# Optimization experiments

Hardware: AMD Instinct MI355X
Metric: run time of the kernel (lower is better)

## Reference

```python
import jax, jax.numpy as jnp
import numpy as np

B, S, D, H, L, V, F = 4, 2048, 512, 8, 4, 32000, 512
EPS = 1e-3  # keras BatchNormalization default epsilon


def setup_inputs() -> dict:
    key = jax.random.key(0)
    ks = jax.random.split(key, 32)
    n = lambda k, shp, sc=0.02: (jax.random.normal(k, shp, jnp.float32) * sc)
    inp = {
        "sequence": jax.random.randint(ks[0], (B, S), 0, V, dtype=jnp.int32),
        # padding mask: 1 for kept tokens, 0 for padded; broadcast over [B,h,S,S]
        "padding_mask": (jax.random.uniform(ks[1], (B, 1, 1, S)) > 0.1).astype(jnp.float32),
        "pos_embeddings": n(ks[2], (S, D), 1.0),
        "emb": n(ks[3], (V, D), 1.0),
        "wq": n(ks[4], (L, D, D)), "bq": jnp.zeros((L, D), jnp.float32),
        "wk": n(ks[5], (L, D, D)), "bk": jnp.zeros((L, D), jnp.float32),
        "wv": n(ks[6], (L, D, D)), "bv": jnp.zeros((L, D), jnp.float32),
        "wo": n(ks[7], (L, D, D)), "bo": jnp.zeros((L, D), jnp.float32),
        "an_gamma": 1.0 + n(ks[8], (L, D)), "an_beta": n(ks[9], (L, D)),
        "an_mean": n(ks[10], (L, D), 0.1), "an_var": 0.5 + jax.random.uniform(ks[11], (L, D)),
        "d1_w": n(ks[12], (L, D, F)), "d1_b": jnp.zeros((L, F), jnp.float32),
        "d2_w": n(ks[13], (L, F, D)), "d2_b": jnp.zeros((L, D), jnp.float32),
        "fn_gamma": 1.0 + n(ks[14], (L, D)), "fn_beta": n(ks[15], (L, D)),
        "fn_mean": n(ks[16], (L, D), 0.1), "fn_var": 0.5 + jax.random.uniform(ks[17], (L, D)),
    }
    return inp


def _bn(x, gamma, beta, mean, var):
    # keras BatchNormalization in inference mode (moving statistics), axis=-1
    return (x - mean) * jax.lax.rsqrt(var + EPS) * gamma + beta


def reference(sequence, padding_mask, pos_embeddings, emb,
              wq, bq, wk, bk, wv, bv, wo, bo,
              an_gamma, an_beta, an_mean, an_var,
              d1_w, d1_b, d2_w, d2_b,
              fn_gamma, fn_beta, fn_mean, fn_var):
    b, s = sequence.shape
    nlayers, d, _ = wq.shape
    h = H
    dk = d // h
    scale = 1.0 / jnp.sqrt(jnp.float32(dk))

    x = emb[sequence] + pos_embeddings[:s, :]  # [B,S,D]

    def split_heads(t):  # [B,S,D] -> [B,h,S,dk]
        return t.reshape(b, s, h, dk).transpose(0, 2, 1, 3)

    for i in range(nlayers):
        q = split_heads(x @ wq[i] + bq[i])
        k = split_heads(x @ wk[i] + bk[i])
        v = split_heads(x @ wv[i] + bv[i])
        score = jnp.einsum('bhqd,bhkd->bhqk', q, k) * scale  # [B,h,S,S]
        if padding_mask is not None:
            score = score * padding_mask
            score = jnp.where(score == 0, jnp.float32(-1e9), score)
        align = jax.nn.softmax(score, axis=-1)
        ctx = jnp.einsum('bhqk,bhkd->bhqd', align, v)
        ctx = ctx.transpose(0, 2, 1, 3).reshape(b, s, d)
        heads = ctx @ wo[i] + bo[i]
        sub = _bn(x + heads, an_gamma[i], an_beta[i], an_mean[i], an_var[i])
        ffn = jax.nn.relu(sub @ d1_w[i] + d1_b[i]) @ d2_w[i] + d2_b[i]
        x = _bn(sub + ffn, fn_gamma[i], fn_beta[i], fn_mean[i], fn_var[i])
    return x
```

## Files before the change

kernel.cpp:

```cpp
#include <hip/hip_runtime.h>
#include <stdint.h>
#include <stddef.h>

constexpr int BB = 4, SS = 2048, DD = 512, HH = 8, LL = 4;
constexpr int NTOK = BB * SS;
constexpr float BN_EPS = 1e-3f;

using bh = __bf16;
typedef __bf16 bf16x8 __attribute__((ext_vector_type(8)));
typedef float  f32x4  __attribute__((ext_vector_type(4)));

#define DEV __device__ __forceinline__
#define WAITVM(n) asm volatile("s_waitcnt vmcnt(" #n ")" ::: "memory")
#define WAITLGKM0 asm volatile("s_waitcnt lgkmcnt(0)" ::: "memory")

DEV void gload_lds16(const void* g, void* l) {
    __builtin_amdgcn_global_load_lds(
        (const __attribute__((address_space(1))) void*)g,
        (__attribute__((address_space(3))) void*)l, 16, 0, 0);
}

__global__ void wprep(const float* __restrict__ in, bh* __restrict__ out, int ostride) {
    __shared__ float t[32][33];
    const float* ip = in + (size_t)blockIdx.z * DD * DD;
    bh* op = out + (size_t)blockIdx.z * ostride;
    const int r0 = blockIdx.y * 32, c0 = blockIdx.x * 32;
    const int tx = threadIdx.x, ty = threadIdx.y;
    #pragma unroll
    for (int i = ty; i < 32; i += 8) t[i][tx] = ip[(size_t)(r0 + i) * DD + c0 + tx];
    __syncthreads();
    #pragma unroll
    for (int i = ty; i < 32; i += 8) op[(size_t)(c0 + i) * DD + r0 + tx] = (bh)t[tx][i];
}

__global__ void maskprep(const float* __restrict__ mask, float* __restrict__ mb) {
    const int i = ((int)blockIdx.x * 256 + threadIdx.x) * 4;
    const float4 m4 = *(const float4*)(mask + i);
    float4 o;
    o.x = (m4.x == 0.f) ? -1e30f : 0.f;
    o.y = (m4.y == 0.f) ? -1e30f : 0.f;
    o.z = (m4.z == 0.f) ? -1e30f : 0.f;
    o.w = (m4.w == 0.f) ? -1e30f : 0.f;
    *(float4*)(mb + i) = o;
}

__global__ void embed_k(const int* __restrict__ seq, const float* __restrict__ emb,
                        const float* __restrict__ pos, bh* __restrict__ xb) {
    const int m = blockIdx.x;
    const int s = m & (SS - 1);
    const int tok = seq[m];
    const int d = threadIdx.x * 4;
    const float4 e  = *(const float4*)(emb + (size_t)tok * DD + d);
    const float4 pz = *(const float4*)(pos + (size_t)s * DD + d);
    union { bh h[4]; uint64_t u; } pk;
    pk.h[0] = (bh)(e.x + pz.x); pk.h[1] = (bh)(e.y + pz.y);
    pk.h[2] = (bh)(e.z + pz.z); pk.h[3] = (bh)(e.w + pz.w);
    *(uint64_t*)(xb + (size_t)m * DD + d) = pk.u;
}

template <int EP, bool WF32>
__global__ __launch_bounds__(256, 4)
void gemm64(const bh* __restrict__ A, const bh* __restrict__ Bt,
            const float* __restrict__ bias, bh* __restrict__ outb,
            const bh* __restrict__ resb, float* __restrict__ Xo,
            const float* __restrict__ gamma, const float* __restrict__ beta,
            const float* __restrict__ mean, const float* __restrict__ var) {
    constexpr int BK = 64, NKT = DD / BK;
    __shared__ __align__(16) bh As[2][64 * BK];
    __shared__ __align__(16) bh Bs[2][64 * BK];

    const int tid = threadIdx.x;
    const int w = tid >> 6, lane = tid & 63;
    const int l15 = lane & 15, l4 = lane >> 4;
    const int i = (int)blockIdx.x;
    const int xcd = i & 7, j = i >> 3;
    const int bm = xcd * 16 + (j >> 3);
    const int bn = j & 7;
    const int m0 = bm * 64, n0 = bn * 64;
    const int wr = w >> 1, wc = w & 1;

    f32x4 acc[2][2] = {};
    const int sr = lane >> 3;
    const int cbx = (lane & 7) ^ sr;

    auto stage = [&](int buf, int kk) {
        #pragma unroll
        for (int ii = 0; ii < 2; ++ii) {
            const int idx = w * 2 + ii;
            const int r = idx * 8 + sr;
            gload_lds16(A + (size_t)(m0 + r) * DD + kk + 8 * cbx, &As[buf][idx * 512]);
            gload_lds16(Bt + (size_t)(n0 + r) * DD + kk + 8 * cbx, &Bs[buf][idx * 512]);
        }
    };

    stage(0, 0);
    __syncthreads();

    for (int kt = 0; kt < NKT; ++kt) {
        const int buf = kt & 1;
        if (kt > 0) { WAITVM(0); __builtin_amdgcn_s_barrier(); }
        if (kt + 1 < NKT) stage(buf ^ 1, (kt + 1) * BK);

        const char* Ab = (const char*)&As[buf][0];
        const char* Bb = (const char*)&Bs[buf][0];
        #pragma unroll
        for (int ks = 0; ks < 2; ++ks) {
            bf16x8 af[2], bfr[2];
            const int cby = ks * 64 + l4 * 16;
            #pragma unroll
            for (int mf = 0; mf < 2; ++mf) {
                const int row = wr * 32 + mf * 16 + l15;
                af[mf] = *(const bf16x8*)(Ab + row * 128 + (cby ^ ((row & 7) << 4)));
            }
            #pragma unroll
            for (int nf = 0; nf < 2; ++nf) {
                const int row = wc * 32 + nf * 16 + l15;
                bfr[nf] = *(const bf16x8*)(Bb + row * 128 + (cby ^ ((row & 7) << 4)));
            }
            __builtin_amdgcn_s_setprio(1);
            #pragma unroll
            for (int mf = 0; mf < 2; ++mf)
                #pragma unroll
                for (int nf = 0; nf < 2; ++nf)
                    acc[mf][nf] = __builtin_amdgcn_mfma_f32_16x16x32_bf16(
                        af[mf], bfr[nf], acc[mf][nf], 0, 0, 0);
            __builtin_amdgcn_s_setprio(0);
        }
    }

    #pragma unroll
    for (int nf = 0; nf < 2; ++nf) {
        const int n = n0 + wc * 32 + nf * 16 + l15;
        const float bi = bias[n];
        float g = 0.f, be = 0.f, mu = 0.f, iv = 0.f;
        if constexpr (EP == 1) {
            g = gamma[n]; be = beta[n]; mu = mean[n];
            iv = rsqrtf(var[n] + BN_EPS);
        }
        #pragma unroll
        for (int mf = 0; mf < 2; ++mf) {
            #pragma unroll
            for (int r = 0; r < 4; ++r) {
                const int m = m0 + wr * 32 + mf * 16 + l4 * 4 + r;
                const size_t off = (size_t)m * DD + n;
                const float v = acc[mf][nf][r] + bi;
                if constexpr (EP == 2) {
                    outb[off] = (bh)fmaxf(v, 0.f);
                } else {
                    const float t = (float)resb[off] + v;
                    const float s = (t - mu) * iv * g + be;
                    outb[off] = (bh)s;
                    if constexpr (WF32) Xo[off] = s;
                }
            }
        }
    }
}

__global__ __launch_bounds__(256, 3)
void gemm_qkv(const bh* __restrict__ A, const bh* __restrict__ Bt,
              const float* __restrict__ bq, const float* __restrict__ bk,
              const float* __restrict__ bv,
              bh* __restrict__ qb, bh* __restrict__ kb, bh* __restrict__ vT) {
    constexpr int BM = 128, BN = 64, BK = 64, NKT = DD / BK;
    __shared__ __align__(16) bh As[2][BM * BK];
    __shared__ __align__(16) bh Bs[2][BN * BK];

    const int tid = threadIdx.x;
    const int w = tid >> 6, lane = tid & 63;
    const int l15 = lane & 15, l4 = lane >> 4;
    const int i = (int)blockIdx.x;
    const int xcd = i & 7, j = i >> 3;
    const int bm = xcd * 8 + (j & 7);
    const int bn = j >> 3;
    const int m0 = bm * BM, n0 = bn * BN;
    const int wr = w >> 1, wc = w & 1;

    f32x4 acc[4][2] = {};
    const int sr = lane >> 3;
    const int cbx = (lane & 7) ^ sr;

    auto stage = [&](int buf, int kk) {
        #pragma unroll
        for (int ii = 0; ii < 4; ++ii) {
            const int idx = w * 4 + ii;
            const int r = idx * 8 + sr;
            gload_lds16(A + (size_t)(m0 + r) * DD + kk + 8 * cbx, &As[buf][idx * 512]);
        }
        #pragma unroll
        for (int ii = 0; ii < 2; ++ii) {
            const int idx = w * 2 + ii;
            const int r = idx * 8 + sr;
            gload_lds16(Bt + (size_t)(n0 + r) * DD + kk + 8 * cbx, &Bs[buf][idx * 512]);
        }
    };

    stage(0, 0);
    stage(1, BK);

    for (int kt = 0; kt < NKT; ++kt) {
        const int buf = kt & 1;
        if (kt + 1 < NKT) { WAITVM(6); } else { WAITVM(0); }
        __builtin_amdgcn_s_barrier();

        const char* Ab = (const char*)&As[buf][0];
        const char* Bb = (const char*)&Bs[buf][0];
        #pragma unroll
        for (int ks = 0; ks < 2; ++ks) {
            bf16x8 af[4], bfr[2];
            const int cby = ks * 64 + l4 * 16;
            #pragma unroll
            for (int mf = 0; mf < 4; ++mf) {
                const int row = wr * 64 + mf * 16 + l15;
                af[mf] = *(const bf16x8*)(Ab + row * 128 + (cby ^ ((row & 7) << 4)));
            }
            #pragma unroll
            for (int nf = 0; nf < 2; ++nf) {
                const int row = wc * 32 + nf * 16 + l15;
                bfr[nf] = *(const bf16x8*)(Bb + row * 128 + (cby ^ ((row & 7) << 4)));
            }
            #pragma unroll
            for (int mf = 0; mf < 4; ++mf)
                #pragma unroll
                for (int nf = 0; nf < 2; ++nf)
                    acc[mf][nf] = __builtin_amdgcn_mfma_f32_16x16x32_bf16(
                        af[mf], bfr[nf], acc[mf][nf], 0, 0, 0);
        }
        WAITLGKM0;
        __builtin_amdgcn_s_barrier();
        if (kt + 2 < NKT) stage(buf, (kt + 2) * BK);
    }

    const int part = n0 >> 9;
    #pragma unroll
    for (int nf = 0; nf < 2; ++nf) {
        const int n = n0 + wc * 32 + nf * 16 + l15;
        const int nn = n & 511;
        const float bi = (part == 0 ? bq : part == 1 ? bk : bv)[nn];
        if (part < 2) {
            bh* out = part ? kb : qb;
            #pragma unroll
            for (int mf = 0; mf < 4; ++mf)
                #pragma unroll
                for (int r = 0; r < 4; ++r) {
                    const int m = m0 + wr * 64 + mf * 16 + l4 * 4 + r;
                    out[(size_t)m * DD + nn] = (bh)(acc[mf][nf][r] + bi);
                }
        } else {
            const int hh = nn >> 6, dk = nn & 63;
            #pragma unroll
            for (int mf = 0; mf < 4; ++mf) {
                const int m = m0 + wr * 64 + mf * 16 + l4 * 4;
                const int bb2 = m >> 11, s = m & (SS - 1);
                union { bh h4[4]; uint64_t u; } pk;
                #pragma unroll
                for (int r = 0; r < 4; ++r)
                    pk.h4[r] = (bh)(acc[mf][nf][r] + bi);
                *(uint64_t*)(vT + ((size_t)((bb2 * HH + hh) * 64) + dk) * SS + s) = pk.u;
            }
        }
    }
}

__global__ __launch_bounds__(256, 4)
void flash_attn(const bh* __restrict__ Q, const bh* __restrict__ K,
                const bh* __restrict__ VT, const float* __restrict__ mb,
                bh* __restrict__ O) {
    constexpr int KVB = 32, NT = SS / KVB;
    constexpr float CSC = 0.18033688f;
    __shared__ __align__(16) bh Ks[2][KVB * 64];
    __shared__ __align__(16) bh Vs[2][64 * KVB];
    __shared__ __align__(16) bh Plds[4][16 * 40];

    const int tid = threadIdx.x;
    const int w = tid >> 6, lane = tid & 63;
    const int l15 = lane & 15, l4 = lane >> 4;

    const int i = (int)blockIdx.x;
    const int xcd = i & 7, j = i >> 3;
    const int g = xcd * 4 + (j >> 5);
    const int qt = j & 31;
    const int h = g & 7, b = g >> 3;

    const int q0 = qt * 64 + w * 16;

    const bh* qp = Q + (size_t)(b * SS + q0 + l15) * DD + h * 64 + l4 * 8;
    const bf16x8 qf0 = *(const bf16x8*)qp;
    const bf16x8 qf1 = *(const bf16x8*)(qp + 32);

    f32x4 ctx[4] = {};
    f32x4 accl = {};
    float m2 = -3e38f;

    bf16x8 ones;
    #pragma unroll
    for (int z = 0; z < 8; ++z) ones[z] = (bh)1.0f;

    const int ksr = lane >> 3;
    const int kcb = (lane & 7) ^ ksr;
    const int vrow = lane >> 2;
    const int vcb  = (lane & 3) ^ (vrow & 3);

    const bh* kg = K + ((size_t)(b * SS) + w * 8 + ksr) * DD + h * 64 + 8 * kcb;
    const bh* vg = VT + ((size_t)((b * HH + h) * 64) + w * 16 + vrow) * SS + 8 * vcb;
    const float* mbb = mb + (size_t)b * SS + l4 * 4;

    auto stage = [&](int buf, int kt) {
        gload_lds16(kg + (size_t)kt * DD, &Ks[buf][w * 512]);
        gload_lds16(vg + kt,              &Vs[buf][w * 512]);
    };

    f32x4 mbc[2];
    stage(0, 0);
    mbc[0] = *(const f32x4*)(mbb);
    mbc[1] = *(const f32x4*)(mbb + 16);
    __syncthreads();

    for (int t = 0; t < NT; ++t) {
        const int buf = t & 1;
        const int kt = t * KVB;
        if (t > 0) { WAITVM(2); __builtin_amdgcn_s_barrier(); }
        if (t + 1 < NT) stage(buf ^ 1, kt + KVB);

        const char* Kb = (const char*)&Ks[buf][0];
        bf16x8 kf[2][2];
        #pragma unroll
        for (int ks = 0; ks < 2; ++ks)
            #pragma unroll
            for (int nf = 0; nf < 2; ++nf) {
                const int row = nf * 16 + l15;
                kf[ks][nf] = *(const bf16x8*)(Kb + row * 128 +
                              ((ks * 64 + l4 * 16) ^ ((row & 7) << 4)));
            }
        f32x4 sc[2] = {};
        __builtin_amdgcn_s_setprio(1);
        #pragma unroll
        for (int ks = 0; ks < 2; ++ks)
            #pragma unroll
            for (int nf = 0; nf < 2; ++nf)
                sc[nf] = __builtin_amdgcn_mfma_f32_16x16x32_bf16(
                    kf[ks][nf], ks ? qf1 : qf0, sc[nf], 0, 0, 0);
        __builtin_amdgcn_s_setprio(0);

        float tm = -3e38f;
        #pragma unroll
        for (int nf = 0; nf < 2; ++nf)
            #pragma unroll
            for (int r = 0; r < 4; ++r) {
                const float z = fmaf(sc[nf][r], CSC, mbc[nf][r]);
                sc[nf][r] = z;
                tm = fmaxf(tm, z);
            }
        if (__any(tm > m2 + 11.5f)) {
            tm = fmaxf(tm, __shfl_xor(tm, 16, 64));
            tm = fmaxf(tm, __shfl_xor(tm, 32, 64));
            const float mn = fmaxf(fmaxf(tm, m2), -60.f);
            const float fac = __builtin_amdgcn_exp2f(m2 - mn);
            m2 = mn;
            accl *= fac;
            #pragma unroll
            for (int nf = 0; nf < 4; ++nf)
                #pragma unroll
                for (int r = 0; r < 4; ++r)
                    ctx[nf][r] *= fac;
        }

        char* Pw = (char*)&Plds[w][0] + l15 * 80;
        #pragma unroll
        for (int nf = 0; nf < 2; ++nf) {
            union { bh h4[4]; uint64_t u; } pk;
            #pragma unroll
            for (int r = 0; r < 4; ++r)
                pk.h4[r] = (bh)__builtin_amdgcn_exp2f(sc[nf][r] - m2);
            *(uint64_t*)(Pw + nf * 32 + l4 * 8) = pk.u;
        }
        WAITLGKM0;
        const bf16x8 pa = *(const bf16x8*)(Pw + l4 * 16);

        const char* Vb = (const char*)&Vs[buf][0];
        bf16x8 vf[4];
        #pragma unroll
        for (int nf = 0; nf < 4; ++nf) {
            const int row = nf * 16 + l15;
            vf[nf] = *(const bf16x8*)(Vb + row * 64 + ((l4 ^ (l15 & 3)) << 4));
        }
        __builtin_amdgcn_s_setprio(1);
        #pragma unroll
        for (int nf = 0; nf < 4; ++nf)
            ctx[nf] = __builtin_amdgcn_mfma_f32_16x16x32_bf16(vf[nf], pa, ctx[nf], 0, 0, 0);
        accl = __builtin_amdgcn_mfma_f32_16x16x32_bf16(ones, pa, accl, 0, 0, 0);
        __builtin_amdgcn_s_setprio(0);

        if (t + 1 < NT) {
            mbc[0] = *(const f32x4*)(mbb + kt + KVB);
            mbc[1] = *(const f32x4*)(mbb + kt + KVB + 16);
        }
    }

    const float linv = 1.0f / accl[0];
    #pragma unroll
    for (int nf = 0; nf < 4; ++nf) {
        union { bh h4[4]; uint64_t u; } pk;
        #pragma unroll
        for (int r = 0; r < 4; ++r)
            pk.h4[r] = (bh)(ctx[nf][r] * linv);
        *(uint64_t*)(O + (size_t)(b * SS + q0 + l15) * DD +
                     h * 64 + nf * 16 + l4 * 4) = pk.u;
    }
}

extern "C" void kernel_launch(void* const* d_in, const int* in_sizes, int n_in,
                              void* d_out, int out_size, void* d_ws, size_t ws_size,
                              hipStream_t stream) {
    const int*   seq  = (const int*)  d_in[0];
    const float* mask = (const float*)d_in[1];
    const float* pos  = (const float*)d_in[2];
    const float* emb  = (const float*)d_in[3];
    const float* wq = (const float*)d_in[4];  const float* bq = (const float*)d_in[5];
    const float* wk = (const float*)d_in[6];  const float* bk = (const float*)d_in[7];
    const float* wv = (const float*)d_in[8];  const float* bv = (const float*)d_in[9];
    const float* wo = (const float*)d_in[10]; const float* bo = (const float*)d_in[11];
    const float* ag = (const float*)d_in[12]; const float* ab = (const float*)d_in[13];
    const float* am = (const float*)d_in[14]; const float* av = (const float*)d_in[15];
    const float* d1w = (const float*)d_in[16]; const float* d1b = (const float*)d_in[17];
    const float* d2w = (const float*)d_in[18]; const float* d2b = (const float*)d_in[19];
    const float* fg = (const float*)d_in[20]; const float* fb = (const float*)d_in[21];
    const float* fm = (const float*)d_in[22]; const float* fv = (const float*)d_in[23];

    float* X = (float*)d_out;

    char* p = (char*)d_ws;
    auto take = [&](size_t n) { char* q = p; p += (n + 255) & ~(size_t)255; return q; };
    const size_t WE  = (size_t)LL * DD * DD;
    const size_t WQE = (size_t)LL * 3 * DD * DD;
    bh* wcat = (bh*)take(WQE * 2);
    bh* wot = (bh*)take(WE * 2);
    bh* w1t = (bh*)take(WE * 2);
    bh* w2t = (bh*)take(WE * 2);
    const size_t AE = (size_t)NTOK * DD;
    bh* xb   = (bh*)take(AE * 2);
    bh* qb   = (bh*)take(AE * 2);
    bh* kb   = (bh*)take(AE * 2);
    bh* ctxb = (bh*)take(AE * 2);
    bh* subb = (bh*)take(AE * 2);
    bh* h1b  = (bh*)take(AE * 2);
    bh* vT   = (bh*)take(AE * 2);
    float* mbias = (float*)take((size_t)BB * SS * 4);

    const int QKV_OS = 3 * DD * DD;
    const dim3 wg(16, 16, LL), wb(32, 8);
    wprep<<<wg, wb, 0, stream>>>(wq,  wcat + 0 * DD * DD, QKV_OS);
    wprep<<<wg, wb, 0, stream>>>(wk,  wcat + 1 * DD * DD, QKV_OS);
    wprep<<<wg, wb, 0, stream>>>(wv,  wcat + 2 * DD * DD, QKV_OS);
    wprep<<<wg, wb, 0, stream>>>(wo,  wot, DD * DD);
    wprep<<<wg, wb, 0, stream>>>(d1w, w1t, DD * DD);
    wprep<<<wg, wb, 0, stream>>>(d2w, w2t, DD * DD);

    maskprep<<<dim3(BB * SS / 1024), dim3(256), 0, stream>>>(mask, mbias);
    embed_k<<<dim3(NTOK), dim3(128), 0, stream>>>(seq, emb, pos, xb);

    for (int l = 0; l < LL; ++l) {
        const size_t wof = (size_t)l * DD * DD;
        const int    bof = l * DD;
        gemm_qkv<<<dim3(1536), dim3(256), 0, stream>>>(
            xb, wcat + (size_t)l * QKV_OS, bq + bof, bk + bof, bv + bof, qb, kb, vT);
        flash_attn<<<dim3(1024), dim3(256), 0, stream>>>(qb, kb, vT, mbias, ctxb);
        gemm64<1, false><<<dim3(1024), dim3(256), 0, stream>>>(
            ctxb, wot + wof, bo + bof, subb, xb, nullptr,
            ag + bof, ab + bof, am + bof, av + bof);
        gemm64<2, false><<<dim3(1024), dim3(256), 0, stream>>>(
            subb, w1t + wof, d1b + bof, h1b, nullptr, nullptr,
            nullptr, nullptr, nullptr, nullptr);
        if (l + 1 < LL) {
            gemm64<1, false><<<dim3(1024), dim3(256), 0, stream>>>(
                h1b, w2t + wof, d2b + bof, xb, subb, nullptr,
                fg + bof, fb + bof, fm + bof, fv + bof);
        } else {
            gemm64<1, true><<<dim3(1024), dim3(256), 0, stream>>>(
                h1b, w2t + wof, d2b + bof, xb, subb, X,
                fg + bof, fb + bof, fm + bof, fv + bof);
        }
    }
}
```

Before: 467.9 us.

## Restructure attention to two Q subtiles per wave, register-load GEMM B operand

Flash attention now runs 2 waves per block, each handling 32 query rows as two 16-row subtiles, so every K/V tile staged into LDS is reused across twice as many queries per wave. The epilogue GEMMs stop staging B through LDS: each wave loads its B fragments straight into registers, and A moves to a three-buffer LDS pipeline with partial vmcnt waits so the next tiles stay in flight during compute. The six weight-prep launches are merged into one kernel. The cost is higher register pressure in both kernels and uncoalesced direct global loads for B, which may lower occupancy.

```diff
diff --git a/kernel.cpp b/kernel.cpp
--- a/kernel.cpp
+++ b/kernel.cpp
@@ -13,6 +13,7 @@
 #define DEV __device__ __forceinline__
 #define WAITVM(n) asm volatile("s_waitcnt vmcnt(" #n ")" ::: "memory")
 #define WAITLGKM0 asm volatile("s_waitcnt lgkmcnt(0)" ::: "memory")
+#define MEMBAR    asm volatile("" ::: "memory")
 
 DEV void gload_lds16(const void* g, void* l) {
     __builtin_amdgcn_global_load_lds(
@@ -20,17 +21,33 @@
         (__attribute__((address_space(3))) void*)l, 16, 0, 0);
 }
 
-__global__ void wprep(const float* __restrict__ in, bh* __restrict__ out, int ostride) {
+__global__ void wprep_all(const float* __restrict__ wq, const float* __restrict__ wk,
+                          const float* __restrict__ wv, const float* __restrict__ wo,
+                          const float* __restrict__ d1, const float* __restrict__ d2,
+                          bh* __restrict__ wcat, bh* __restrict__ wot,
+                          bh* __restrict__ w1t, bh* __restrict__ w2t) {
     __shared__ float t[32][33];
-    const float* ip = in + (size_t)blockIdx.z * DD * DD;
-    bh* op = out + (size_t)blockIdx.z * ostride;
+    const int z = blockIdx.z;
+    const int m = z >> 2, l = z & 3;
+    constexpr int QOS = 3 * DD * DD;
+    const float* src;
+    bh* dst;
+    switch (m) {
+        case 0:  src = wq; dst = wcat + (size_t)l * QOS;               break;
+        case 1:  src = wk; dst = wcat + (size_t)l * QOS + DD * DD;     break;
+        case 2:  src = wv; dst = wcat + (size_t)l * QOS + 2 * DD * DD; break;
+        case 3:  src = wo; dst = wot + (size_t)l * DD * DD;            break;
+        case 4:  src = d1; dst = w1t + (size_t)l * DD * DD;            break;
+        default: src = d2; dst = w2t + (size_t)l * DD * DD;            break;
+    }
+    src += (size_t)l * DD * DD;
     const int r0 = blockIdx.y * 32, c0 = blockIdx.x * 32;
     const int tx = threadIdx.x, ty = threadIdx.y;
     #pragma unroll
-    for (int i = ty; i < 32; i += 8) t[i][tx] = ip[(size_t)(r0 + i) * DD + c0 + tx];
+    for (int i = ty; i < 32; i += 8) t[i][tx] = src[(size_t)(r0 + i) * DD + c0 + tx];
     __syncthreads();
     #pragma unroll
-    for (int i = ty; i < 32; i += 8) op[(size_t)(c0 + i) * DD + r0 + tx] = (bh)t[tx][i];
+    for (int i = ty; i < 32; i += 8) dst[(size_t)(c0 + i) * DD + r0 + tx] = (bh)t[tx][i];
 }
 
 __global__ void maskprep(const float* __restrict__ mask, float* __restrict__ mb) {
@@ -60,14 +77,13 @@
 
 template <int EP, bool WF32>
 __global__ __launch_bounds__(256, 4)
-void gemm64(const bh* __restrict__ A, const bh* __restrict__ Bt,
-            const float* __restrict__ bias, bh* __restrict__ outb,
-            const bh* __restrict__ resb, float* __restrict__ Xo,
-            const float* __restrict__ gamma, const float* __restrict__ beta,
-            const float* __restrict__ mean, const float* __restrict__ var) {
+void gemm_ep(const bh* __restrict__ A, const bh* __restrict__ Bt,
+             const float* __restrict__ bias, bh* __restrict__ outb,
+             const bh* __restrict__ resb, float* __restrict__ Xo,
+             const float* __restrict__ gamma, const float* __restrict__ beta,
+             const float* __restrict__ mean, const float* __restrict__ var) {
     constexpr int BK = 64, NKT = DD / BK;
-    __shared__ __align__(16) bh As[2][64 * BK];
-    __shared__ __align__(16) bh Bs[2][64 * BK];
+    __shared__ __align__(16) bh As[3][64 * BK];
 
     const int tid = threadIdx.x;
     const int w = tid >> 6, lane = tid & 63;
@@ -83,48 +99,67 @@
     const int sr = lane >> 3;
     const int cbx = (lane & 7) ^ sr;
 
-    auto stage = [&](int buf, int kk) {
+    auto stageA = [&](int buf, int kk) {
         #pragma unroll
         for (int ii = 0; ii < 2; ++ii) {
             const int idx = w * 2 + ii;
             const int r = idx * 8 + sr;
             gload_lds16(A + (size_t)(m0 + r) * DD + kk + 8 * cbx, &As[buf][idx * 512]);
-            gload_lds16(Bt + (size_t)(n0 + r) * DD + kk + 8 * cbx, &Bs[buf][idx * 512]);
         }
     };
 
-    stage(0, 0);
-    __syncthreads();
-
+    const bh* bg = Bt + (size_t)(n0 + wc * 32 + l15) * DD + l4 * 8;
+    bf16x8 bqA[2][2], bqB[2][2];
+
+    stageA(0, 0);
+    #pragma unroll
+    for (int ks = 0; ks < 2; ++ks)
+        #pragma unroll
+        for (int nf = 0; nf < 2; ++nf)
+            bqA[ks][nf] = *(const bf16x8*)(bg + nf * 16 * DD + ks * 32);
+    MEMBAR;
+    stageA(1, BK);
+    #pragma unroll
+    for (int ks = 0; ks < 2; ++ks)
+        #pragma unroll
+        for (int nf = 0; nf < 2; ++nf)
+            bqB[ks][nf] = *(const bf16x8*)(bg + nf * 16 * DD + BK + ks * 32);
+    MEMBAR;
+
+    #pragma unroll
     for (int kt = 0; kt < NKT; ++kt) {
-        const int buf = kt & 1;
-        if (kt > 0) { WAITVM(0); __builtin_amdgcn_s_barrier(); }
-        if (kt + 1 < NKT) stage(buf ^ 1, (kt + 1) * BK);
-
-        const char* Ab = (const char*)&As[buf][0];
-        const char* Bb = (const char*)&Bs[buf][0];
+        if (kt < NKT - 1) { WAITVM(6); } else { WAITVM(0); }
+        __builtin_amdgcn_s_barrier();
+
+        bf16x8 (*bq)[2] = (kt & 1) ? bqB : bqA;
+        const char* Ab = (const char*)&As[kt % 3][0];
         #pragma unroll
         for (int ks = 0; ks < 2; ++ks) {
-            bf16x8 af[2], bfr[2];
+            bf16x8 af[2];
             const int cby = ks * 64 + l4 * 16;
             #pragma unroll
             for (int mf = 0; mf < 2; ++mf) {
                 const int row = wr * 32 + mf * 16 + l15;
                 af[mf] = *(const bf16x8*)(Ab + row * 128 + (cby ^ ((row & 7) << 4)));
             }
-            #pragma unroll
-            for (int nf = 0; nf < 2; ++nf) {
-                const int row = wc * 32 + nf * 16 + l15;
-                bfr[nf] = *(const bf16x8*)(Bb + row * 128 + (cby ^ ((row & 7) << 4)));
-            }
             __builtin_amdgcn_s_setprio(1);
             #pragma unroll
             for (int mf = 0; mf < 2; ++mf)
                 #pragma unroll
                 for (int nf = 0; nf < 2; ++nf)
                     acc[mf][nf] = __builtin_amdgcn_mfma_f32_16x16x32_bf16(
-                        af[mf], bfr[nf], acc[mf][nf], 0, 0, 0);
+                        af[mf], bq[ks][nf], acc[mf][nf], 0, 0, 0);
             __builtin_amdgcn_s_setprio(0);
+        }
+
+        if (kt + 2 < NKT) {
+            stageA((kt + 2) % 3, (kt + 2) * BK);
+            bf16x8 (*bqn)[2] = (kt & 1) ? bqB : bqA;
+            #pragma unroll
+            for (int ks = 0; ks < 2; ++ks)
+                #pragma unroll
+                for (int nf = 0; nf < 2; ++nf)
+                    bqn[ks][nf] = *(const bf16x8*)(bg + nf * 16 * DD + (kt + 2) * BK + ks * 32);
         }
     }
 
@@ -262,7 +297,7 @@
     }
 }
 
-__global__ __launch_bounds__(256, 4)
+__global__ __launch_bounds__(128, 2)
 void flash_attn(const bh* __restrict__ Q, const bh* __restrict__ K,
                 const bh* __restrict__ VT, const float* __restrict__ mb,
                 bh* __restrict__ O) {
@@ -270,7 +305,7 @@
     constexpr float CSC = 0.18033688f;
     __shared__ __align__(16) bh Ks[2][KVB * 64];
     __shared__ __align__(16) bh Vs[2][64 * KVB];
-    __shared__ __align__(16) bh Plds[4][16 * 40];
+    __shared__ __align__(16) bh Plds[2][2][16 * 40];
 
     const int tid = threadIdx.x;
     const int w = tid >> 6, lane = tid & 63;
@@ -282,15 +317,19 @@
     const int qt = j & 31;
     const int h = g & 7, b = g >> 3;
 
-    const int q0 = qt * 64 + w * 16;
-
-    const bh* qp = Q + (size_t)(b * SS + q0 + l15) * DD + h * 64 + l4 * 8;
-    const bf16x8 qf0 = *(const bf16x8*)qp;
-    const bf16x8 qf1 = *(const bf16x8*)(qp + 32);
-
-    f32x4 ctx[4] = {};
-    f32x4 accl = {};
-    float m2 = -3e38f;
+    const int q0 = qt * 64 + w * 32;
+
+    bf16x8 qf[2][2];
+    #pragma unroll
+    for (int st = 0; st < 2; ++st) {
+        const bh* qp = Q + (size_t)(b * SS + q0 + st * 16 + l15) * DD + h * 64 + l4 * 8;
+        qf[st][0] = *(const bf16x8*)qp;
+        qf[st][1] = *(const bf16x8*)(qp + 32);
+    }
+
+    f32x4 ctx[2][4] = {};
+    f32x4 accl[2] = {};
+    float m2[2] = {-3e38f, -3e38f};
 
     bf16x8 ones;
     #pragma unroll
@@ -301,13 +340,17 @@
     const int vrow = lane >> 2;
     const int vcb  = (lane & 3) ^ (vrow & 3);
 
-    const bh* kg = K + ((size_t)(b * SS) + w * 8 + ksr) * DD + h * 64 + 8 * kcb;
-    const bh* vg = VT + ((size_t)((b * HH + h) * 64) + w * 16 + vrow) * SS + 8 * vcb;
+    const bh* kg = K + ((size_t)(b * SS) + ksr) * DD + h * 64 + 8 * kcb;
+    const bh* vg = VT + ((size_t)((b * HH + h) * 64) + vrow) * SS + 8 * vcb;
     const float* mbb = mb + (size_t)b * SS + l4 * 4;
 
     auto stage = [&](int buf, int kt) {
-        gload_lds16(kg + (size_t)kt * DD, &Ks[buf][w * 512]);
-        gload_lds16(vg + kt,              &Vs[buf][w * 512]);
+        #pragma unroll
+        for (int ii = 0; ii < 2; ++ii) {
+            const int idx = w * 2 + ii;
+            gload_lds16(kg + (size_t)(kt + idx * 8) * DD, &Ks[buf][idx * 512]);
+            gload_lds16(vg + (size_t)(idx * 16) * SS + kt, &Vs[buf][idx * 512]);
+        }
     };
 
     f32x4 mbc[2];
@@ -332,50 +375,57 @@
                 kf[ks][nf] = *(const bf16x8*)(Kb + row * 128 +
                               ((ks * 64 + l4 * 16) ^ ((row & 7) << 4)));
             }
-        f32x4 sc[2] = {};
+        f32x4 sc[2][2] = {};
         __builtin_amdgcn_s_setprio(1);
         #pragma unroll
         for (int ks = 0; ks < 2; ++ks)
             #pragma unroll
+            for (int st = 0; st < 2; ++st)
+                #pragma unroll
+                for (int nf = 0; nf < 2; ++nf)
+                    sc[st][nf] = __builtin_amdgcn_mfma_f32_16x16x32_bf16(
+                        kf[ks][nf], qf[st][ks], sc[st][nf], 0, 0, 0);
+        __builtin_amdgcn_s_setprio(0);
+
+        #pragma unroll
+        for (int st = 0; st < 2; ++st) {
+            float tm = -3e38f;
+            #pragma unroll
             for (int nf = 0; nf < 2; ++nf)
-                sc[nf] = __builtin_amdgcn_mfma_f32_16x16x32_bf16(
-                    kf[ks][nf], ks ? qf1 : qf0, sc[nf], 0, 0, 0);
-        __builtin_amdgcn_s_setprio(0);
-
-        float tm = -3e38f;
-        #pragma unroll
-        for (int nf = 0; nf < 2; ++nf)
-            #pragma unroll
-            for (int r = 0; r < 4; ++r) {
-                const float z = fmaf(sc[nf][r], CSC, mbc[nf][r]);
-                sc[nf][r] = z;
-                tm = fmaxf(tm, z);
-            }
-        if (__any(tm > m2 + 11.5f)) {
-            tm = fmaxf(tm, __shfl_xor(tm, 16, 64));
-            tm = fmaxf(tm, __shfl_xor(tm, 32, 64));
-            const float mn = fmaxf(fmaxf(tm, m2), -60.f);
-            const float fac = __builtin_amdgcn_exp2f(m2 - mn);
-            m2 = mn;
-            accl *= fac;
-            #pragma unroll
-            for (int nf = 0; nf < 4; ++nf)
+                #pragma unroll
+                for (int r = 0; r < 4; ++r) {
+                    const float z = fmaf(sc[st][nf][r], CSC, mbc[nf][r]);
+                    sc[st][nf][r] = z;
+                    tm = fmaxf(tm, z);
+                }
+            if (__any(tm > m2[st] + 11.5f)) {
+                tm = fmaxf(tm, __shfl_xor(tm, 16, 64));
+                tm = fmaxf(tm, __shfl_xor(tm, 32, 64));
+                const float mn = fmaxf(fmaxf(tm, m2[st]), -60.f);
+                const float fac = __builtin_amdgcn_exp2f(m2[st] - mn);
+                m2[st] = mn;
+                accl[st] *= fac;
+                #pragma unroll
+                for (int nf = 0; nf < 4; ++nf)
+                    #pragma unroll
+                    for (int r = 0; r < 4; ++r)
+                        ctx[st][nf][r] *= fac;
+            }
+            char* Pw = (char*)&Plds[w][st][0] + l15 * 80;
+            #pragma unroll
+            for (int nf = 0; nf < 2; ++nf) {
+                union { bh h4[4]; uint64_t u; } pk;
                 #pragma unroll
                 for (int r = 0; r < 4; ++r)
-                    ctx[nf][r] *= fac;
-        }
-
-        char* Pw = (char*)&Plds[w][0] + l15 * 80;
-        #pragma unroll
-        for (int nf = 0; nf < 2; ++nf) {
-            union { bh h4[4]; uint64_t u; } pk;
-            #pragma unroll
-            for (int r = 0; r < 4; ++r)
-                pk.h4[r] = (bh)__builtin_amdgcn_exp2f(sc[nf][r] - m2);
-            *(uint64_t*)(Pw + nf * 32 + l4 * 8) = pk.u;
+                    pk.h4[r] = (bh)__builtin_amdgcn_exp2f(sc[st][nf][r] - m2[st]);
+                *(uint64_t*)(Pw + nf * 32 + l4 * 8) = pk.u;
+            }
         }
         WAITLGKM0;
-        const bf16x8 pa = *(const bf16x8*)(Pw + l4 * 16);
+        bf16x8 pa[2];
+        #pragma unroll
+        for (int st = 0; st < 2; ++st)
+            pa[st] = *(const bf16x8*)((const char*)&Plds[w][st][0] + l15 * 80 + l4 * 16);
 
         const char* Vb = (const char*)&Vs[buf][0];
         bf16x8 vf[4];
@@ -386,9 +436,14 @@
         }
         __builtin_amdgcn_s_setprio(1);
         #pragma unroll
-        for (int nf = 0; nf < 4; ++nf)
-            ctx[nf] = __builtin_amdgcn_mfma_f32_16x16x32_bf16(vf[nf], pa, ctx[nf], 0, 0, 0);
-        accl = __builtin_amdgcn_mfma_f32_16x16x32_bf16(ones, pa, accl, 0, 0, 0);
+        for (int st = 0; st < 2; ++st) {
+            #pragma unroll
+            for (int nf = 0; nf < 4; ++nf)
+                ctx[st][nf] = __builtin_amdgcn_mfma_f32_16x16x32_bf16(
+                    vf[nf], pa[st], ctx[st][nf], 0, 0, 0);
+            accl[st] = __builtin_amdgcn_mfma_f32_16x16x32_bf16(
+                ones, pa[st], accl[st], 0, 0, 0);
+        }
         __builtin_amdgcn_s_setprio(0);
 
         if (t + 1 < NT) {
@@ -397,15 +452,18 @@
         }
     }
 
-    const float linv = 1.0f / accl[0];
-    #pragma unroll
-    for (int nf = 0; nf < 4; ++nf) {
-        union { bh h4[4]; uint64_t u; } pk;
-        #pragma unroll
-        for (int r = 0; r < 4; ++r)
-            pk.h4[r] = (bh)(ctx[nf][r] * linv);
-        *(uint64_t*)(O + (size_t)(b * SS + q0 + l15) * DD +
-                     h * 64 + nf * 16 + l4 * 4) = pk.u;
+    #pragma unroll
+    for (int st = 0; st < 2; ++st) {
+        const float linv = 1.0f / accl[st][0];
+        #pragma unroll
+        for (int nf = 0; nf < 4; ++nf) {
+            union { bh h4[4]; uint64_t u; } pk;
+            #pragma unroll
+            for (int r = 0; r < 4; ++r)
+                pk.h4[r] = (bh)(ctx[st][nf][r] * linv);
+            *(uint64_t*)(O + (size_t)(b * SS + q0 + st * 16 + l15) * DD +
+                         h * 64 + nf * 16 + l4 * 4) = pk.u;
+        }
     }
 }
 
@@ -448,13 +506,8 @@
     float* mbias = (float*)take((size_t)BB * SS * 4);
 
     const int QKV_OS = 3 * DD * DD;
-    const dim3 wg(16, 16, LL), wb(32, 8);
-    wprep<<<wg, wb, 0, stream>>>(wq,  wcat + 0 * DD * DD, QKV_OS);
-    wprep<<<wg, wb, 0, stream>>>(wk,  wcat + 1 * DD * DD, QKV_OS);
-    wprep<<<wg, wb, 0, stream>>>(wv,  wcat + 2 * DD * DD, QKV_OS);
-    wprep<<<wg, wb, 0, stream>>>(wo,  wot, DD * DD);
-    wprep<<<wg, wb, 0, stream>>>(d1w, w1t, DD * DD);
-    wprep<<<wg, wb, 0, stream>>>(d2w, w2t, DD * DD);
+    wprep_all<<<dim3(16, 16, 24), dim3(32, 8), 0, stream>>>(
+        wq, wk, wv, wo, d1w, d2w, wcat, wot, w1t, w2t);
 
     maskprep<<<dim3(BB * SS / 1024), dim3(256), 0, stream>>>(mask, mbias);
     embed_k<<<dim3(NTOK), dim3(128), 0, stream>>>(seq, emb, pos, xb);
@@ -464,19 +517,19 @@
         const int    bof = l * DD;
         gemm_qkv<<<dim3(1536), dim3(256), 0, stream>>>(
             xb, wcat + (size_t)l * QKV_OS, bq + bof, bk + bof, bv + bof, qb, kb, vT);
-        flash_attn<<<dim3(1024), dim3(256), 0, stream>>>(qb, kb, vT, mbias, ctxb);
-        gemm64<1, false><<<dim3(1024), dim3(256), 0, stream>>>(
+        flash_attn<<<dim3(1024), dim3(128), 0, stream>>>(qb, kb, vT, mbias, ctxb);
+        gemm_ep<1, false><<<dim3(1024), dim3(256), 0, stream>>>(
             ctxb, wot + wof, bo + bof, subb, xb, nullptr,
             ag + bof, ab + bof, am + bof, av + bof);
-        gemm64<2, false><<<dim3(1024), dim3(256), 0, stream>>>(
+        gemm_ep<2, false><<<dim3(1024), dim3(256), 0, stream>>>(
             subb, w1t + wof, d1b + bof, h1b, nullptr, nullptr,
             nullptr, nullptr, nullptr, nullptr);
         if (l + 1 < LL) {
-            gemm64<1, false><<<dim3(1024), dim3(256), 0, stream>>>(
+            gemm_ep<1, false><<<dim3(1024), dim3(256), 0, stream>>>(
                 h1b, w2t + wof, d2b + bof, xb, subb, nullptr,
                 fg + bof, fb + bof, fm + bof, fv + bof);
         } else {
-            gemm64<1, true><<<dim3(1024), dim3(256), 0, stream>>>(
+            gemm_ep<1, true><<<dim3(1024), dim3(256), 0, stream>>>(
                 h1b, w2t + wof, d2b + bof, xb, subb, X,
                 fg + bof, fb + bof, fm + bof, fv + bof);
         }
```

Result: slower. 604.9 us (+29.3%).
